# Optimization experiments

Measured on AMD Instinct MI355X. Metric: run time of the kernel, lower is better.

## Reference

```python
import jax, jax.numpy as jnp
import numpy as np

MARGIN = 0.3
EPS = 1e-12


def setup_inputs() -> dict:
    key = jax.random.key(0)
    k1, k2 = jax.random.split(key)
    n, d = 4096, 1024
    inputs = jax.random.normal(k1, (n, d), dtype=jnp.float32)
    targets = jax.random.randint(k2, (n,), 0, 64, dtype=jnp.int64)
    return {"inputs": inputs, "targets": targets}


def reference(inputs, targets):
    n = inputs.shape[0]
    # pairwise Euclidean distance matrix: ||xi||^2 + ||xj||^2 - 2 xi.xj
    sq = jnp.sum(inputs * inputs, axis=1)  # [n]
    dist2 = sq[:, None] + sq[None, :] - 2.0 * (inputs @ inputs.T)
    dist = jnp.sqrt(jnp.clip(dist2, EPS))  # [n, n]
    # same-label mask (includes diagonal, matching original)
    mask = targets[:, None] == targets[None, :]
    # fused masked row-wise hard mining
    neg_inf = jnp.asarray(-jnp.inf, dist.dtype)
    pos_inf = jnp.asarray(jnp.inf, dist.dtype)
    dist_ap = jnp.max(jnp.where(mask, dist, neg_inf), axis=1)  # hardest positive
    dist_an = jnp.min(jnp.where(mask, pos_inf, dist), axis=1)  # hardest negative
    # MarginRankingLoss with y=1: mean(relu(margin - (dist_an - dist_ap)))
    loss = jnp.mean(jnp.maximum(MARGIN - (dist_an - dist_ap), 0.0))
    prec = jnp.sum((dist_an > dist_ap).astype(jnp.float32)) / n
    return (loss, prec)
```

## Files before the change

### kernel.cpp

```cpp
#include <hip/hip_runtime.h>
#include <stdint.h>

#define MARGIN 0.3f
#define EPS 1e-12f

typedef __attribute__((ext_vector_type(8))) __bf16 bf16x8;
typedef __attribute__((ext_vector_type(4))) float f32x4;

__device__ __forceinline__ unsigned short f2bf(float f) {
    unsigned u = __float_as_uint(f);
    unsigned r = (u + 0x7FFFu + ((u >> 16) & 1u)) >> 16;
    return (unsigned short)r;
}

#define GLD16(gp, lp)                                                     \
    __builtin_amdgcn_global_load_lds(                                     \
        (const __attribute__((address_space(1))) void*)(gp),              \
        (__attribute__((address_space(3))) void*)(lp), 16, 0, 0)

__global__ __launch_bounds__(256) void prep_kernel(
    const float* __restrict__ X, unsigned short* __restrict__ Xbf,
    float* __restrict__ sqg, unsigned* __restrict__ apb,
    unsigned* __restrict__ anb, unsigned* __restrict__ ctr, int d) {
    const int wave = threadIdx.x >> 6, lane = threadIdx.x & 63;
    const int row = blockIdx.x * 4 + wave;
    const float4* Xr = (const float4*)(X + (size_t)row * d);
    ushort4* Or = (ushort4*)(Xbf + (size_t)row * d);
    float s = 0.0f;
    const int nq = d >> 2;
    for (int i = lane; i < nq; i += 64) {
        float4 v = Xr[i];
        s += v.x * v.x + v.y * v.y + v.z * v.z + v.w * v.w;
        ushort4 o;
        o.x = f2bf(v.x); o.y = f2bf(v.y); o.z = f2bf(v.z); o.w = f2bf(v.w);
        Or[i] = o;
    }
    for (int off = 32; off > 0; off >>= 1) s += __shfl_down(s, off, 64);
    if (lane == 0) {
        sqg[row] = s;
        apb[row] = 0u;
        anb[row] = 0x7F800000u;
    }
    if (blockIdx.x == 0 && threadIdx.x == 0) ctr[0] = 0u;
}

#define BM 128
#define BN 128
#define BK 32

__global__ __launch_bounds__(512, 4) void tri_gemm(
    const unsigned short* __restrict__ Xbf, const float* __restrict__ sqg,
    const int* __restrict__ tgt, unsigned* __restrict__ apb,
    unsigned* __restrict__ anb, unsigned* __restrict__ ctr,
    float* __restrict__ out, int n, int d, int nblk) {
    __shared__ unsigned short ldsA[2][BM * BK];
    __shared__ unsigned short ldsB[2][BN * BK];

    const int tid  = threadIdx.x;
    const int lane = tid & 63;
    const int wave = tid >> 6;
    const int wm = wave >> 2;
    const int wn = wave & 3;
    const int lo = lane & 15, hi = lane >> 4;

    const int orig = blockIdx.x;
    const int q = nblk >> 3, r = nblk & 7;
    const int xcd = orig & 7, idx = orig >> 3;
    const int bid = (xcd < r ? xcd * (q + 1) : r * (q + 1) + (xcd - r) * q) + idx;

    int bi = (int)((sqrtf(8.0f * (float)bid + 1.0f) - 1.0f) * 0.5f);
    while ((bi + 1) * (bi + 2) / 2 <= bid) ++bi;
    while (bi * (bi + 1) / 2 > bid) --bi;
    const int bj = bid - bi * (bi + 1) / 2;
    const int rowBase = bi * BM;
    const int colBase = bj * BN;
    const bool offdiag = (bi != bj);

    const int lrow = lane >> 2;
    const int lk   = (lane & 3) * 8;
    const unsigned short* gA0 = Xbf + (size_t)(rowBase + wave * 16 + lrow) * d + lk;
    const unsigned short* gB0 = Xbf + (size_t)(colBase + wave * 16 + lrow) * d + lk;

    f32x4 acc[4][2] = {};

    const int nt = d / BK;
    int cur = 0;
    GLD16(gA0, &ldsA[0][wave * 512]);
    GLD16(gB0, &ldsB[0][wave * 512]);
    asm volatile("s_waitcnt vmcnt(0)" ::: "memory");
    __syncthreads();

    for (int t = 0; t < nt; ++t) {
        if (t + 1 < nt) {
            const int k0 = (t + 1) * BK;
            GLD16(gA0 + k0, &ldsA[cur ^ 1][wave * 512]);
            GLD16(gB0 + k0, &ldsB[cur ^ 1][wave * 512]);
        }
        bf16x8 a[4], b[2];
#pragma unroll
        for (int mi = 0; mi < 4; ++mi)
            a[mi] = *(const bf16x8*)&ldsA[cur][(wm * 64 + mi * 16 + lo) * BK + hi * 8];
#pragma unroll
        for (int ni = 0; ni < 2; ++ni)
            b[ni] = *(const bf16x8*)&ldsB[cur][(wn * 32 + ni * 16 + lo) * BK + hi * 8];
#pragma unroll
        for (int mi = 0; mi < 4; ++mi)
#pragma unroll
            for (int ni = 0; ni < 2; ++ni)
                acc[mi][ni] = __builtin_amdgcn_mfma_f32_16x16x32_bf16(
                    a[mi], b[ni], acc[mi][ni], 0, 0, 0);
        if (t + 1 < nt) {
            asm volatile("s_waitcnt vmcnt(0)" ::: "memory");
            __syncthreads();
            cur ^= 1;
        }
    }

    float sqj[2];
    int   tj[2];
#pragma unroll
    for (int ni = 0; ni < 2; ++ni) {
        const int gj = colBase + wn * 32 + ni * 16 + lo;
        sqj[ni] = sqg[gj];
        tj[ni]  = tgt[gj];
    }
    float cap[2], can[2];
#pragma unroll
    for (int ni = 0; ni < 2; ++ni) { cap[ni] = 0.0f; can[ni] = __uint_as_float(0x7F800000u); }

#pragma unroll
    for (int mi = 0; mi < 4; ++mi) {
#pragma unroll
        for (int j = 0; j < 4; ++j) {
            const int gi = rowBase + wm * 64 + mi * 16 + hi * 4 + j;
            const float sqi = sqg[gi];
            const int   ti  = tgt[gi];
            float ap = 0.0f;
            float an = __uint_as_float(0x7F800000u);
#pragma unroll
            for (int ni = 0; ni < 2; ++ni) {
                const float d2 = sqi + sqj[ni] - 2.0f * acc[mi][ni][j];
                const float dist = sqrtf(fmaxf(d2, EPS));
                if (ti == tj[ni]) {
                    ap = fmaxf(ap, dist);
                    cap[ni] = fmaxf(cap[ni], dist);
                } else {
                    an = fminf(an, dist);
                    can[ni] = fminf(can[ni], dist);
                }
            }
#pragma unroll
            for (int m = 1; m < 16; m <<= 1) {
                ap = fmaxf(ap, __shfl_xor(ap, m, 64));
                an = fminf(an, __shfl_xor(an, m, 64));
            }
            if (lo == 0) {
                atomicMax(&apb[gi], __float_as_uint(ap));
                atomicMin(&anb[gi], __float_as_uint(an));
            }
        }
    }
    if (offdiag) {
#pragma unroll
        for (int ni = 0; ni < 2; ++ni) {
            float ap = cap[ni], an = can[ni];
#pragma unroll
            for (int m = 16; m < 64; m <<= 1) {
                ap = fmaxf(ap, __shfl_xor(ap, m, 64));
                an = fminf(an, __shfl_xor(an, m, 64));
            }
            if (hi == 0) {
                const int gj = colBase + wn * 32 + ni * 16 + lo;
                atomicMax(&apb[gj], __float_as_uint(ap));
                atomicMin(&anb[gj], __float_as_uint(an));
            }
        }
    }

    __threadfence();
    __syncthreads();
    __shared__ int lastFlag;
    if (tid == 0) {
        unsigned prev = __hip_atomic_fetch_add(ctr, 1u, __ATOMIC_ACQ_REL,
                                               __HIP_MEMORY_SCOPE_AGENT);
        lastFlag = (prev == (unsigned)(nblk - 1)) ? 1 : 0;
    }
    __syncthreads();
    if (lastFlag) {
        float ls = 0.0f, pc = 0.0f;
        for (int i = tid; i < n; i += 512) {
            const float ap = __uint_as_float(__hip_atomic_load(
                &apb[i], __ATOMIC_RELAXED, __HIP_MEMORY_SCOPE_AGENT));
            const float an = __uint_as_float(__hip_atomic_load(
                &anb[i], __ATOMIC_RELAXED, __HIP_MEMORY_SCOPE_AGENT));
            ls += fmaxf(MARGIN - (an - ap), 0.0f);
            pc += (an > ap) ? 1.0f : 0.0f;
        }
        __shared__ float rl[8], rp[8];
        for (int off = 32; off > 0; off >>= 1) {
            ls += __shfl_down(ls, off, 64);
            pc += __shfl_down(pc, off, 64);
        }
        if ((tid & 63) == 0) { rl[tid >> 6] = ls; rp[tid >> 6] = pc; }
        __syncthreads();
        if (tid == 0) {
            float L = 0.0f, P = 0.0f;
#pragma unroll
            for (int w = 0; w < 8; ++w) { L += rl[w]; P += rp[w]; }
            out[0] = L / (float)n;
            out[1] = P / (float)n;
        }
    }
}

__global__ __launch_bounds__(256) void fb_zero(float* __restrict__ out) {
    if (threadIdx.x == 0) { out[0] = 0.0f; out[1] = 0.0f; }
}

__global__ __launch_bounds__(256) void fb_row(
    const float* __restrict__ X, const int* __restrict__ tgt,
    float* __restrict__ out, int n, int d) {
    __shared__ float xi[4096];
    const int i = blockIdx.x;
    const int tid = threadIdx.x;
    for (int k = tid; k < d; k += 256) xi[k] = X[(size_t)i * d + k];
    __syncthreads();
    const int ti = tgt[i];
    float ap = 0.0f;
    float an = __uint_as_float(0x7F800000u);
    for (int j = tid; j < n; j += 256) {
        const float4* Xj = (const float4*)(X + (size_t)j * d);
        float s = 0.0f;
        for (int k4 = 0; k4 < (d >> 2); ++k4) {
            float4 v = Xj[k4];
            float4 u = *(const float4*)&xi[k4 * 4];
            float dx = u.x - v.x, dy = u.y - v.y, dz = u.z - v.z, dw = u.w - v.w;
            s += dx * dx + dy * dy + dz * dz + dw * dw;
        }
        const float dist = sqrtf(fmaxf(s, EPS));
        if (tgt[j] == ti) ap = fmaxf(ap, dist);
        else              an = fminf(an, dist);
    }
    for (int m = 1; m < 64; m <<= 1) {
        ap = fmaxf(ap, __shfl_xor(ap, m, 64));
        an = fminf(an, __shfl_xor(an, m, 64));
    }
    __shared__ float rap[4], ran[4];
    const int wave = tid >> 6, lane = tid & 63;
    if (lane == 0) { rap[wave] = ap; ran[wave] = an; }
    __syncthreads();
    if (tid == 0) {
        ap = fmaxf(fmaxf(rap[0], rap[1]), fmaxf(rap[2], rap[3]));
        an = fminf(fminf(ran[0], ran[1]), fminf(ran[2], ran[3]));
        atomicAdd(&out[0], fmaxf(MARGIN - (an - ap), 0.0f));
        atomicAdd(&out[1], (an > ap) ? 1.0f : 0.0f);
    }
}

__global__ __launch_bounds__(64) void fb_scale(float* __restrict__ out, float inv_n) {
    if (threadIdx.x == 0) { out[0] *= inv_n; out[1] *= inv_n; }
}

extern "C" void kernel_launch(void* const* d_in, const int* in_sizes, int n_in,
                              void* d_out, int out_size, void* d_ws, size_t ws_size,
                              hipStream_t stream) {
    const float* X   = (const float*)d_in[0];
    const int*   tgt = (const int*)d_in[1];
    const int n = in_sizes[1];
    const int d = in_sizes[0] / n;

    const size_t need = (size_t)n * d * 2 + (size_t)n * 4 * 3 + 4;
    if (ws_size >= need) {
        char* ws = (char*)d_ws;
        unsigned short* Xbf = (unsigned short*)ws;
        float*    sqg = (float*)(ws + (size_t)n * d * 2);
        unsigned* apb = (unsigned*)((char*)sqg + (size_t)n * 4);
        unsigned* anb = apb + n;
        unsigned* ctr = anb + n;

        const int nb = n / BM;
        const int nblk = nb * (nb + 1) / 2;
        prep_kernel<<<n / 4, 256, 0, stream>>>(X, Xbf, sqg, apb, anb, ctr, d);
        tri_gemm<<<nblk, 512, 0, stream>>>(Xbf, sqg, tgt, apb, anb, ctr,
                                           (float*)d_out, n, d, nblk);
    } else {
        fb_zero<<<1, 256, 0, stream>>>((float*)d_out);
        fb_row<<<n, 256, 0, stream>>>(X, tgt, (float*)d_out, n, d);
        fb_scale<<<1, 64, 0, stream>>>((float*)d_out, 1.0f / (float)n);
    }
}
```

Measured before the change: 176.2 us.

## Enlarge GEMM tile to 256x128 with rectangular triangular tiling and partial vmcnt pipelining

```diff
diff --git a/kernel.cpp b/kernel.cpp
--- a/kernel.cpp
+++ b/kernel.cpp
@@ -44,7 +44,7 @@
     if (blockIdx.x == 0 && threadIdx.x == 0) ctr[0] = 0u;
 }
 
-#define BM 128
+#define BM 256
 #define BN 128
 #define BK 32
 
@@ -59,8 +59,8 @@
     const int tid  = threadIdx.x;
     const int lane = tid & 63;
     const int wave = tid >> 6;
-    const int wm = wave >> 2;
-    const int wn = wave & 3;
+    const int wm = wave >> 1;
+    const int wn = wave & 1;
     const int lo = lane & 15, hi = lane >> 4;
 
     const int orig = blockIdx.x;
@@ -68,65 +68,67 @@
     const int xcd = orig & 7, idx = orig >> 3;
     const int bid = (xcd < r ? xcd * (q + 1) : r * (q + 1) + (xcd - r) * q) + idx;
 
-    int bi = (int)((sqrtf(8.0f * (float)bid + 1.0f) - 1.0f) * 0.5f);
-    while ((bi + 1) * (bi + 2) / 2 <= bid) ++bi;
-    while (bi * (bi + 1) / 2 > bid) --bi;
-    const int bj = bid - bi * (bi + 1) / 2;
+    int bi = (int)((sqrtf(4.0f * (float)bid + 1.0f) - 1.0f) * 0.5f);
+    while ((bi + 1) * (bi + 2) <= bid) ++bi;
+    while (bi * (bi + 1) > bid) --bi;
+    const int bj = bid - bi * (bi + 1);
     const int rowBase = bi * BM;
     const int colBase = bj * BN;
-    const bool offdiag = (bi != bj);
 
     const int lrow = lane >> 2;
     const int lk   = (lane & 3) * 8;
     const unsigned short* gA0 = Xbf + (size_t)(rowBase + wave * 16 + lrow) * d + lk;
+    const unsigned short* gA1 = gA0 + (size_t)128 * d;
     const unsigned short* gB0 = Xbf + (size_t)(colBase + wave * 16 + lrow) * d + lk;
 
-    f32x4 acc[4][2] = {};
+#define STAGE(bufi, k0)                                                   \
+    do {                                                                  \
+        GLD16(gA0 + (k0), &ldsA[bufi][wave * 512]);                       \
+        GLD16(gA1 + (k0), &ldsA[bufi][(8 + wave) * 512]);                 \
+        GLD16(gB0 + (k0), &ldsB[bufi][wave * 512]);                       \
+    } while (0)
+
+    f32x4 acc[4][4] = {};
 
     const int nt = d / BK;
     int cur = 0;
-    GLD16(gA0, &ldsA[0][wave * 512]);
-    GLD16(gB0, &ldsB[0][wave * 512]);
-    asm volatile("s_waitcnt vmcnt(0)" ::: "memory");
-    __syncthreads();
-
+    STAGE(0, 0);
     for (int t = 0; t < nt; ++t) {
         if (t + 1 < nt) {
-            const int k0 = (t + 1) * BK;
-            GLD16(gA0 + k0, &ldsA[cur ^ 1][wave * 512]);
-            GLD16(gB0 + k0, &ldsB[cur ^ 1][wave * 512]);
-        }
-        bf16x8 a[4], b[2];
+            STAGE(cur ^ 1, (t + 1) * BK);
+            asm volatile("s_waitcnt vmcnt(3)" ::: "memory");
+        } else {
+            asm volatile("s_waitcnt vmcnt(0)" ::: "memory");
+        }
+        asm volatile("s_barrier" ::: "memory");
+        bf16x8 a[4], b[4];
 #pragma unroll
         for (int mi = 0; mi < 4; ++mi)
             a[mi] = *(const bf16x8*)&ldsA[cur][(wm * 64 + mi * 16 + lo) * BK + hi * 8];
 #pragma unroll
-        for (int ni = 0; ni < 2; ++ni)
-            b[ni] = *(const bf16x8*)&ldsB[cur][(wn * 32 + ni * 16 + lo) * BK + hi * 8];
+        for (int ni = 0; ni < 4; ++ni)
+            b[ni] = *(const bf16x8*)&ldsB[cur][(wn * 64 + ni * 16 + lo) * BK + hi * 8];
 #pragma unroll
         for (int mi = 0; mi < 4; ++mi)
 #pragma unroll
-            for (int ni = 0; ni < 2; ++ni)
+            for (int ni = 0; ni < 4; ++ni)
                 acc[mi][ni] = __builtin_amdgcn_mfma_f32_16x16x32_bf16(
                     a[mi], b[ni], acc[mi][ni], 0, 0, 0);
-        if (t + 1 < nt) {
-            asm volatile("s_waitcnt vmcnt(0)" ::: "memory");
-            __syncthreads();
-            cur ^= 1;
-        }
-    }
-
-    float sqj[2];
-    int   tj[2];
-#pragma unroll
-    for (int ni = 0; ni < 2; ++ni) {
-        const int gj = colBase + wn * 32 + ni * 16 + lo;
+        asm volatile("s_barrier" ::: "memory");
+        cur ^= 1;
+    }
+
+    float sqj[4];
+    int   tj[4];
+#pragma unroll
+    for (int ni = 0; ni < 4; ++ni) {
+        const int gj = colBase + wn * 64 + ni * 16 + lo;
         sqj[ni] = sqg[gj];
         tj[ni]  = tgt[gj];
     }
-    float cap[2], can[2];
-#pragma unroll
-    for (int ni = 0; ni < 2; ++ni) { cap[ni] = 0.0f; can[ni] = __uint_as_float(0x7F800000u); }
+    float cap[4], can[4];
+#pragma unroll
+    for (int ni = 0; ni < 4; ++ni) { cap[ni] = 0.0f; can[ni] = __uint_as_float(0x7F800000u); }
 
 #pragma unroll
     for (int mi = 0; mi < 4; ++mi) {
@@ -138,7 +140,7 @@
             float ap = 0.0f;
             float an = __uint_as_float(0x7F800000u);
 #pragma unroll
-            for (int ni = 0; ni < 2; ++ni) {
+            for (int ni = 0; ni < 4; ++ni) {
                 const float d2 = sqi + sqj[ni] - 2.0f * acc[mi][ni][j];
                 const float dist = sqrtf(fmaxf(d2, EPS));
                 if (ti == tj[ni]) {
@@ -160,20 +162,18 @@
             }
         }
     }
-    if (offdiag) {
-#pragma unroll
-        for (int ni = 0; ni < 2; ++ni) {
-            float ap = cap[ni], an = can[ni];
-#pragma unroll
-            for (int m = 16; m < 64; m <<= 1) {
-                ap = fmaxf(ap, __shfl_xor(ap, m, 64));
-                an = fminf(an, __shfl_xor(an, m, 64));
-            }
-            if (hi == 0) {
-                const int gj = colBase + wn * 32 + ni * 16 + lo;
-                atomicMax(&apb[gj], __float_as_uint(ap));
-                atomicMin(&anb[gj], __float_as_uint(an));
-            }
+#pragma unroll
+    for (int ni = 0; ni < 4; ++ni) {
+        float ap = cap[ni], an = can[ni];
+#pragma unroll
+        for (int m = 16; m < 64; m <<= 1) {
+            ap = fmaxf(ap, __shfl_xor(ap, m, 64));
+            an = fminf(an, __shfl_xor(an, m, 64));
+        }
+        if (hi == 0) {
+            const int gj = colBase + wn * 64 + ni * 16 + lo;
+            atomicMax(&apb[gj], __float_as_uint(ap));
+            atomicMin(&anb[gj], __float_as_uint(an));
         }
     }
 
@@ -270,7 +270,7 @@
     const int d = in_sizes[0] / n;
 
     const size_t need = (size_t)n * d * 2 + (size_t)n * 4 * 3 + 4;
-    if (ws_size >= need) {
+    if (ws_size >= need && (n % BM) == 0 && (d % (2 * BK)) == 0) {
         char* ws = (char*)d_ws;
         unsigned short* Xbf = (unsigned short*)ws;
         float*    sqg = (float*)(ws + (size_t)n * d * 2);
@@ -278,8 +278,8 @@
         unsigned* anb = apb + n;
         unsigned* ctr = anb + n;
 
-        const int nb = n / BM;
-        const int nblk = nb * (nb + 1) / 2;
+        const int nbI = n / BM;
+        const int nblk = nbI * (nbI + 1);
         prep_kernel<<<n / 4, 256, 0, stream>>>(X, Xbf, sqg, apb, anb, ctr, d);
         tri_gemm<<<nblk, 512, 0, stream>>>(Xbf, sqg, tgt, apb, anb, ctr,
                                            (float*)d_out, n, d, nblk);
```

New measurement: 142.7 us. 19.0% less time.
